# Optimization experiments

Measured on AMD Instinct MI355X. Metric: run time of the kernel, lower is better.

## Reference

```python
import jax, jax.numpy as jnp
import numpy as np

KERNEL = (7, 7)
NUM_CH = 4
EPS = 1e-06
ROPE_BASE = 10000.0


def _rel_dist():
    coords = [np.arange(k, dtype=np.float32) - k // 2 for k in KERNEL]
    g = np.meshgrid(*coords, indexing='ij')
    d = np.sqrt(sum(gi ** 2 for gi in g))
    return jnp.asarray(d.reshape(-1)), float(d.max())


def silu(x):
    return x * jax.nn.sigmoid(x)


def rmsnorm(x, w):
    rms = jnp.sqrt(jnp.mean(x * x, axis=-1, keepdims=True) + EPS)
    return x / rms * w


def apply_rope(x):
    # x: (B, L, H, D); positions run over dim -2 (matches torch default)
    H, D = x.shape[-2], x.shape[-1]
    half = D // 2
    pos = jnp.arange(H, dtype=jnp.float32)
    freqs = 1.0 / (ROPE_BASE ** (jnp.arange(half, dtype=x.dtype) / half))
    ang = pos[:, None] * freqs  # (H, half)
    cos, sin = jnp.cos(ang), jnp.sin(ang)
    x1, x2 = x[..., :half], x[..., half:2 * half]
    return jnp.concatenate([x1 * cos - x2 * sin, x1 * sin + x2 * cos], axis=-1)


def unfold2d(x):
    # x: (B, Hs, Ws, C) -> (B, Hs, Ws, k1*k2, C), row-major kernel order
    B, Hs, Ws, C = x.shape
    k1, k2 = KERNEL
    xp = jnp.pad(x, ((0, 0), ((k1 - 1) // 2, k1 // 2), ((k2 - 1) // 2, k2 // 2), (0, 0)))
    wins = [xp[:, i:i + Hs, j:j + Ws, :] for i in range(k1) for j in range(k2)]
    return jnp.stack(wins, axis=3)


def setup_inputs() -> dict:
    key = jax.random.key(0)
    ks = jax.random.split(key, 8)
    C = 256
    x = jax.random.normal(ks[0], (2, 64, 64, C), dtype=jnp.float32)
    W_qkv = jax.random.normal(ks[1], (C, 3 * C), dtype=jnp.float32) * 0.02
    w_qnorm = jnp.ones((C // NUM_CH,), dtype=jnp.float32)
    w_knorm = jnp.ones((C // NUM_CH,), dtype=jnp.float32)
    W_wp = jax.random.normal(ks[2], (C, 2 * NUM_CH), dtype=jnp.float32) * 0.02
    b_wp = jax.random.normal(ks[3], (2 * NUM_CH,), dtype=jnp.float32) * 0.02
    w_onorm = jnp.ones((C,), dtype=jnp.float32)
    W_out = jax.random.normal(ks[4], (C, C), dtype=jnp.float32) * 0.02
    W_gate = jax.random.normal(ks[5], (C, C), dtype=jnp.float32) * 0.02
    b_gate = 2.0 * jnp.ones((C,), dtype=jnp.float32)
    return {"x": x, "W_qkv": W_qkv, "w_qnorm": w_qnorm, "w_knorm": w_knorm,
            "W_wp": W_wp, "b_wp": b_wp, "w_onorm": w_onorm, "W_out": W_out,
            "W_gate": W_gate, "b_gate": b_gate}


def reference(x, W_qkv, w_qnorm, w_knorm, W_wp, b_wp, w_onorm, W_out, W_gate, b_gate):
    rel_dist, max_dist = _rel_dist()
    B, Hs, Ws, C = x.shape
    L = Hs * Ws
    H = NUM_CH
    D = C // H
    Wsz = KERNEL[0] * KERNEL[1]
    scale = D ** (-0.5)

    qkv = silu(x @ W_qkv)
    q, k, v = jnp.split(qkv, 3, axis=-1)

    q_flat = apply_rope(rmsnorm(q.reshape(B, L, H, D), w_qnorm))
    k_flat = apply_rope(rmsnorm(k.reshape(B, L, H, D), w_knorm))
    k = k_flat.reshape(B, Hs, Ws, C)

    wp = silu(x @ W_wp + b_wp)  # (B, Hs, Ws, 2H)
    width_raw, sharp_raw = jnp.split(wp, 2, axis=-1)
    width = jax.nn.sigmoid(width_raw) * max_dist + 0.5
    sharpness = jax.nn.sigmoid(sharp_raw) * 9.5 + 0.5

    k_win = unfold2d(k).reshape(B, L, Wsz, H, D)
    v_win = unfold2d(v).reshape(B, L, Wsz, H, D)

    scores = jnp.einsum('blhd,blwhd->blhw', q_flat, k_win) * scale
    width_f = width.reshape(B, L, H, 1)
    sharp_f = sharpness.reshape(B, L, H, 1)
    soft_mask = jax.nn.sigmoid((width_f - rel_dist) * sharp_f)
    scores = scores - (1.0 - soft_mask) * 10000.0
    attn = jax.nn.softmax(scores, axis=-1)

    out = jnp.einsum('blhw,blwhd->blhd', attn, v_win).reshape(B, Hs, Ws, C)
    out = rmsnorm(out, w_onorm)

    gate = jax.nn.sigmoid(silu(v @ W_gate + b_gate))
    merged = gate * v + (1.0 - gate) * out
    return silu(merged @ W_out)
```

## Files before the change

### kernel.cpp

```cpp
#include <hip/hip_runtime.h>
#include <hip/hip_fp16.h>
#include <math.h>

__device__ __forceinline__ float sigm(float x)  { return 1.0f / (1.0f + __expf(-x)); }
__device__ __forceinline__ float siluf(float x) { return x * sigm(x); }

typedef _Float16 half8  __attribute__((ext_vector_type(8)));
typedef _Float16 half4  __attribute__((ext_vector_type(4)));
typedef float    f32x4  __attribute__((ext_vector_type(4)));
typedef unsigned u32x2  __attribute__((ext_vector_type(2)));

__device__ __forceinline__ void gld16(const void* g, void* l) {
    __builtin_amdgcn_global_load_lds(
        (const __attribute__((address_space(1))) unsigned*)g,
        (__attribute__((address_space(3))) unsigned*)l, 16, 0, 0);
}

template <int N>
__device__ __forceinline__ void wait_vmcnt() {
    if constexpr (N == 0)      asm volatile("s_waitcnt vmcnt(0)" ::: "memory");
    else if constexpr (N == 3) asm volatile("s_waitcnt vmcnt(3)" ::: "memory");
    else if constexpr (N == 5) asm volatile("s_waitcnt vmcnt(5)" ::: "memory");
    else if constexpr (N == 6) asm volatile("s_waitcnt vmcnt(6)" ::: "memory");
}

template <int MI, int AMODE>
__device__ __forceinline__ void gemm_core16(
    const __half* __restrict__ A16,
    const __half* __restrict__ Bhi, const __half* __restrict__ Blo,
    int nbs, int m0, int n0, int t, int koff, f32x4 (&acc)[MI][4])
{
    __shared__ short As[2][MI * 1024], BsHi[2][4096], BsLo[2][4096];
    const int lane = t & 63, wave = t >> 6;
    const int wm = (wave >> 1) * (MI << 4), wn = (wave & 1) << 6;
    const int fr = lane & 15, fq = lane >> 4;
    constexpr int NL = MI / 2 + 4;

    auto stage = [&](int kb, int buf) {
        const int kc = (kb + koff) & 7;
#pragma unroll
        for (int hf = 0; hf < MI / 2; ++hf) {
            const int rr = wave * (MI << 3) + (hf << 4);
            size_t ga;
            if (AMODE == 0)
                ga = (((size_t)(kc * 8192 + m0 + rr)) << 5) + (lane << 3);
            else
                ga = (((size_t)(m0 + rr + (lane >> 2))) << 8) + (kc << 5) + ((lane & 3) << 3);
            gld16(A16 + ga, &As[buf][rr << 5]);
        }
#pragma unroll
        for (int hf = 0; hf < 2; ++hf) {
            const int rr = (wave << 5) + (hf << 4);
            const size_t gb = (((size_t)(kc * nbs + n0 + rr)) << 5) + (lane << 3);
            gld16(Bhi + gb, &BsHi[buf][rr << 5]);
            gld16(Blo + gb, &BsLo[buf][rr << 5]);
        }
    };

    stage(0, 0);
#pragma unroll
    for (int kb = 0; kb < 8; ++kb) {
        const int cur = kb & 1;
        if (kb < 7) {
            stage(kb + 1, cur ^ 1);
            wait_vmcnt<NL>();
        } else {
            wait_vmcnt<0>();
        }
        __builtin_amdgcn_s_barrier();

        half8 a[MI], bh[4], bl[4];
#pragma unroll
        for (int i = 0; i < MI; ++i)
            a[i] = *(const half8*)&As[cur][((wm + (i << 4) + fr) << 5) + (fq << 3)];
#pragma unroll
        for (int i = 0; i < 4; ++i) {
            const int boff = ((wn + (i << 4) + fr) << 5) + (fq << 3);
            bh[i] = *(const half8*)&BsHi[cur][boff];
            bl[i] = *(const half8*)&BsLo[cur][boff];
        }
#pragma unroll
        for (int mi = 0; mi < MI; ++mi)
#pragma unroll
            for (int ni = 0; ni < 4; ++ni) {
                acc[mi][ni] = __builtin_amdgcn_mfma_f32_16x16x32_f16(a[mi], bh[ni], acc[mi][ni], 0, 0, 0);
                acc[mi][ni] = __builtin_amdgcn_mfma_f32_16x16x32_f16(a[mi], bl[ni], acc[mi][ni], 0, 0, 0);
            }

        if (kb < 7) __builtin_amdgcn_s_barrier();
    }
}

__device__ __forceinline__ void gemm_core64(
    const __half* __restrict__ A16,
    const __half* __restrict__ Bhi, const __half* __restrict__ Blo,
    int m0, int n0, int t, int koff, f32x4 (&acc)[4])
{
    __shared__ short As[2][2048], BsHi[2][2048], BsLo[2][2048];
    const int lane = t & 63, wave = t >> 6;
    const int wm = wave << 4;
    const int fr = lane & 15, fq = lane >> 4;

    auto stage = [&](int kb, int buf) {
        const int kc = (kb + koff) & 7;
        const int rr = wave << 4;
        const size_t ga = (((size_t)(m0 + rr + (lane >> 2))) << 8) + (kc << 5) + ((lane & 3) << 3);
        gld16(A16 + ga, &As[buf][rr << 5]);
        const size_t gb = (((size_t)(kc * 256 + n0 + rr)) << 5) + (lane << 3);
        gld16(Bhi + gb, &BsHi[buf][rr << 5]);
        gld16(Blo + gb, &BsLo[buf][rr << 5]);
    };

    stage(0, 0);
#pragma unroll
    for (int kb = 0; kb < 8; ++kb) {
        const int cur = kb & 1;
        if (kb < 7) {
            stage(kb + 1, cur ^ 1);
            wait_vmcnt<3>();
        } else {
            wait_vmcnt<0>();
        }
        __builtin_amdgcn_s_barrier();

        half8 a = *(const half8*)&As[cur][((wm + fr) << 5) + (fq << 3)];
        half8 bh[4], bl[4];
#pragma unroll
        for (int ni = 0; ni < 4; ++ni) {
            const int boff = (((ni << 4) + fr) << 5) + (fq << 3);
            bh[ni] = *(const half8*)&BsHi[cur][boff];
            bl[ni] = *(const half8*)&BsLo[cur][boff];
        }
#pragma unroll
        for (int ni = 0; ni < 4; ++ni) {
            acc[ni] = __builtin_amdgcn_mfma_f32_16x16x32_f16(a, bh[ni], acc[ni], 0, 0, 0);
            acc[ni] = __builtin_amdgcn_mfma_f32_16x16x32_f16(a, bl[ni], acc[ni], 0, 0, 0);
        }

        if (kb < 7) __builtin_amdgcn_s_barrier();
    }
}

__global__ __launch_bounds__(256) void prep_kernel(
    const float* __restrict__ x, const float* __restrict__ Wqkv,
    const float* __restrict__ Wgate, const float* __restrict__ Wout,
    const float* __restrict__ Wwp, const float* __restrict__ bwp,
    __half* __restrict__ xh,
    __half* __restrict__ wqh, __half* __restrict__ wql,
    __half* __restrict__ wgh, __half* __restrict__ wgl,
    __half* __restrict__ woh, __half* __restrict__ wol,
    float* __restrict__ width, float* __restrict__ sharp)
{
    __shared__ float xs[32][260];
    const int t = threadIdx.x;
    const int blk = blockIdx.x;
    if (blk < 256) {
        const int row0 = blk << 5;
        for (int e = t; e < 2048; e += 256) {
            int r = e >> 6, cc = (e & 63) << 2;
            *(float4*)&xs[r][cc] = *(const float4*)&x[(size_t)(row0 + r) * 256 + cc];
        }
        __syncthreads();
        const int r = t >> 3, kb = t & 7;
        __half hibuf[32];
#pragma unroll
        for (int i = 0; i < 32; ++i)
            hibuf[i] = __float2half(xs[r][(kb << 5) + i]);
        const size_t ob = ((size_t)(kb * 8192 + row0 + r)) << 5;
#pragma unroll
        for (int i = 0; i < 4; ++i)
            *(int4*)&xh[ob + (i << 3)] = *(int4*)&hibuf[i << 3];
        float a0 = 0.f, a1 = 0.f, a2 = 0.f, a3 = 0.f;
#pragma unroll 4
        for (int k = 0; k < 256; k += 4) {
            a0 += xs[r][k + 0] * Wwp[(k + 0) * 8 + kb];
            a1 += xs[r][k + 1] * Wwp[(k + 1) * 8 + kb];
            a2 += xs[r][k + 2] * Wwp[(k + 2) * 8 + kb];
            a3 += xs[r][k + 3] * Wwp[(k + 3) * 8 + kb];
        }
        const float acc = (a0 + a1) + (a2 + a3);
        float s = sigm(siluf(acc + bwp[kb]));
        const int row = row0 + r;
        if (kb < 4) width[row * 4 + kb] = s * 4.242640687119285f + 0.5f;
        else        sharp[row * 4 + kb - 4] = s * 9.5f + 0.5f;
    } else {
        const float* W; __half *Whi, *Wlo; int N, nb0, ncnt;
        if (blk < 288)      { W = Wqkv;  Whi = wqh; Wlo = wql; N = 768; nb0 = (blk - 256) * 24; ncnt = 24; }
        else if (blk < 296) { W = Wgate; Whi = wgh; Wlo = wgl; N = 256; nb0 = (blk - 288) * 32; ncnt = 32; }
        else                { W = Wout;  Whi = woh; Wlo = wol; N = 256; nb0 = (blk - 296) * 32; ncnt = 32; }
        for (int j = 0; j < ncnt; ++j)
            xs[j][t] = W[(size_t)t * N + nb0 + j];
        __syncthreads();
        for (int c = t; c < ncnt * 8; c += 256) {
            const int j = c >> 3, kb = c & 7;
            __half hibuf[32], lobuf[32];
#pragma unroll
            for (int i = 0; i < 32; ++i) {
                float v = xs[j][(kb << 5) + i];
                __half hv = __float2half(v);
                hibuf[i] = hv;
                lobuf[i] = __float2half(v - __half2float(hv));
            }
            const size_t ob = ((size_t)(kb * N + nb0 + j)) << 5;
#pragma unroll
            for (int i = 0; i < 4; ++i) {
                *(int4*)&Whi[ob + (i << 3)] = *(int4*)&hibuf[i << 3];
                *(int4*)&Wlo[ob + (i << 3)] = *(int4*)&lobuf[i << 3];
            }
        }
    }
}

__global__ __launch_bounds__(256, 3) void gemm_qkv(
    const __half* __restrict__ xh,
    const __half* __restrict__ wqh, const __half* __restrict__ wql,
    const float* __restrict__ wq, const float* __restrict__ wk,
    __half* __restrict__ qh, __half* __restrict__ kh, __half* __restrict__ vh)
{
    const int t  = threadIdx.x;
    const int m0 = blockIdx.y << 6, n0 = blockIdx.x << 7;
    f32x4 acc[2][4] = {};
    gemm_core16<2, 0>(xh, wqh, wql, 768, m0, n0, t, blockIdx.y & 7, acc);

    const int lane = t & 63, wave = t >> 6;
    const int wm = (wave >> 1) << 5, wn = (wave & 1) << 6;
    const int fr = lane & 15, fq = lane >> 4;
    const int gc0 = n0 + wn;
    const int seg = gc0 >> 8;
    const int h   = (gc0 >> 6) & 3;
    const int hc0 = h << 6;

#pragma unroll
    for (int mi = 0; mi < 2; ++mi)
#pragma unroll
        for (int ni = 0; ni < 4; ++ni)
#pragma unroll
            for (int r = 0; r < 4; ++r)
                acc[mi][ni][r] = siluf(acc[mi][ni][r]);

    if (seg == 2) {
#pragma unroll
        for (int mi = 0; mi < 2; ++mi)
#pragma unroll
            for (int r = 0; r < 4; ++r) {
                const size_t row = m0 + wm + (mi << 4) + (fq << 2) + r;
#pragma unroll
                for (int ni = 0; ni < 4; ++ni)
                    vh[row * 256 + hc0 + (ni << 4) + fr] = __float2half(acc[mi][ni][r]);
            }
    } else {
        const float* wnorm = seg ? wk : wq;
        float wv[4];
#pragma unroll
        for (int ni = 0; ni < 4; ++ni) wv[ni] = wnorm[(ni << 4) + fr];
        float cs[2], sn[2];
#pragma unroll
        for (int j = 0; j < 2; ++j) {
            const int d = (j << 4) + fr;
            const float freq = powf(10000.f, -(float)d * (1.f / 32.f));
            const float ang = (float)h * freq;
            cs[j] = cosf(ang); sn[j] = sinf(ang);
        }
        __half* dstbase = (seg ? kh : qh);
#pragma unroll
        for (int mi = 0; mi < 2; ++mi)
#pragma unroll
            for (int r = 0; r < 4; ++r) {
                float ss = acc[mi][0][r] * acc[mi][0][r] + acc[mi][1][r] * acc[mi][1][r]
                         + acc[mi][2][r] * acc[mi][2][r] + acc[mi][3][r] * acc[mi][3][r];
                ss += __shfl_xor(ss, 1); ss += __shfl_xor(ss, 2);
                ss += __shfl_xor(ss, 4); ss += __shfl_xor(ss, 8);
                const float rinv = 1.f / sqrtf(ss * (1.f / 64.f) + 1e-6f);
                float xv[4];
#pragma unroll
                for (int ni = 0; ni < 4; ++ni) xv[ni] = acc[mi][ni][r] * rinv * wv[ni];
                const float o0 = xv[0] * cs[0] - xv[2] * sn[0];
                const float o2 = xv[0] * sn[0] + xv[2] * cs[0];
                const float o1 = xv[1] * cs[1] - xv[3] * sn[1];
                const float o3 = xv[1] * sn[1] + xv[3] * cs[1];
                const size_t row = m0 + wm + (mi << 4) + (fq << 2) + r;
                __half* dst = dstbase + row * 256 + hc0;
                dst[fr]      = __float2half(o0);
                dst[16 + fr] = __float2half(o1);
                dst[32 + fr] = __float2half(o2);
                dst[48 + fr] = __float2half(o3);
            }
    }
}

__global__ __launch_bounds__(256, 2) void gemm_gate(
    const __half* __restrict__ vh,
    const __half* __restrict__ wgh, const __half* __restrict__ wgl,
    const float* __restrict__ bias, const float* __restrict__ attn_o,
    const float* __restrict__ sumsq4, const float* __restrict__ w_onorm,
    __half* __restrict__ mh)
{
    const int t  = threadIdx.x;
    const int m0 = blockIdx.y << 6, n0 = blockIdx.x << 6;
    f32x4 acc[4] = {};
    gemm_core64(vh, wgh, wgl, m0, n0, t, blockIdx.y & 7, acc);

    const int lane = t & 63, wave = t >> 6;
    const int wm = wave << 4;
    const int fr = lane & 15, fq = lane >> 4;

    float rmsf[4];
#pragma unroll
    for (int r = 0; r < 4; ++r) {
        const int m = m0 + wm + (fq << 2) + r;
        float4 s4 = *(const float4*)&sumsq4[(size_t)m * 4];
        rmsf[r] = 1.f / sqrtf((s4.x + s4.y + s4.z + s4.w) * (1.f / 256.f) + 1e-6f);
    }

#pragma unroll
    for (int ni = 0; ni < 4; ++ni) {
        const int n  = n0 + (ni << 4) + fr;
        const int mb = m0 + wm + (fq << 2);
        const float bb  = bias[n];
        const float won = w_onorm[n];
#pragma unroll
        for (int r = 0; r < 4; ++r) {
            const int m = mb + r;
            const float g  = sigm(siluf(acc[ni][r] + bb));
            const float vv = __half2float(vh[(size_t)m * 256 + n]);
            const float oo = attn_o[(size_t)m * 256 + n] * rmsf[r] * won;
            mh[(size_t)m * 256 + n] = __float2half(g * vv + (1.f - g) * oo);
        }
    }
}

__global__ __launch_bounds__(256, 2) void gemm_out(
    const __half* __restrict__ mh,
    const __half* __restrict__ woh, const __half* __restrict__ wol,
    float* __restrict__ out)
{
    const int t  = threadIdx.x;
    const int m0 = blockIdx.y << 6, n0 = blockIdx.x << 6;
    f32x4 acc[4] = {};
    gemm_core64(mh, woh, wol, m0, n0, t, blockIdx.y & 7, acc);

    const int lane = t & 63, wave = t >> 6;
    const int wm = wave << 4;
    const int fr = lane & 15, fq = lane >> 4;
#pragma unroll
    for (int ni = 0; ni < 4; ++ni) {
        const int n  = n0 + (ni << 4) + fr;
        const int mb = m0 + wm + (fq << 2);
#pragma unroll
        for (int r = 0; r < 4; ++r)
            out[(size_t)(mb + r) * 256 + n] = siluf(acc[ni][r]);
    }
}

#define PT 216

__global__ __launch_bounds__(256, 2) void attn_mfma(
    const __half* __restrict__ qh, const __half* __restrict__ kh,
    const __half* __restrict__ vh, const float* __restrict__ width,
    const float* __restrict__ sharp, float* __restrict__ attn_o,
    float* __restrict__ sumsq4)
{
    __shared__ short smem[27648];
    short* Ksh = smem;
    short* Psh = smem;
    short* Vt  = smem + 13824;

    const int t = threadIdx.x;
    const int lane = t & 63, wave = t >> 6;
    const int fr = lane & 15, fq = lane >> 4;
    const int patch = blockIdx.x, h = blockIdx.y, b = blockIdx.z;
    const int pr0 = (patch >> 3) << 3, pc0 = (patch & 7) << 3;
    const int t0 = (wave * 28) >> 4;

    float wd[4], sh[4]; int lq[4];
#pragma unroll
    for (int r = 0; r < 4; ++r) {
        const int q = (wave << 4) + (fq << 2) + r;
        lq[r] = (pr0 + (q >> 3)) * 64 + pc0 + (q & 7);
        wd[r] = width[((b << 12) + lq[r]) * 4 + h];
        sh[r] = sharp[((b << 12) + lq[r]) * 4 + h];
    }

    const int qrow = (wave << 4) + fr;
    const int lqr = (pr0 + (qrow >> 3)) * 64 + pc0 + (qrow & 7);
    const __half* qptr = qh + (((size_t)(b << 12) + lqr) << 8) + (h << 6) + (fq << 3);
    half8 a0 = *(const half8*)qptr;
    half8 a1 = *(const half8*)(qptr + 32);

    const int srow = t >> 4;
    const int d4 = (t & 15) << 2;
    const size_t cbase = (((size_t)b << 12) * 256) + (size_t)h * 64 + d4;

    u32x2 kb2[13], vb2[13];
#pragma unroll
    for (int p = 0; p < 13; ++p) {
        const int prow = (p << 4) + srow;
        const int pi = prow / 14, pj = prow - pi * 14;
        const int gr = pr0 - 3 + pi, gc = pc0 - 3 + pj;
        const bool ok = (prow < 196) & ((unsigned)gr < 64u) & ((unsigned)gc < 64u);
        const int grc = min(max(gr, 0), 63), gcc = min(max(gc, 0), 63);
        const size_t off = cbase + (size_t)(grc * 64 + gcc) * 256;
        u32x2 kv = *(const u32x2*)(kh + off);
        u32x2 vv = *(const u32x2*)(vh + off);
        const u32x2 z = {0u, 0u};
        kb2[p] = ok ? kv : z;
        vb2[p] = ok ? vv : z;
    }

    const int chunk = d4 >> 3, dlo = d4 & 7;
#pragma unroll
    for (int p = 0; p < 13; ++p) {
        const int prow = (p << 4) + srow;
        *(u32x2*)&Ksh[(prow << 6) + ((chunk ^ (prow & 7)) << 3) + dlo] = kb2[p];
        Vt[(d4)     * PT + prow] = (short)(vb2[p].x & 0xffffu);
        Vt[(d4 + 1) * PT + prow] = (short)(vb2[p].x >> 16);
        Vt[(d4 + 2) * PT + prow] = (short)(vb2[p].y & 0xffffu);
        Vt[(d4 + 3) * PT + prow] = (short)(vb2[p].y >> 16);
    }
    __syncthreads();

    f32x4 sc[8];
#pragma unroll
    for (int tl = 0; tl < 8; ++tl) {
        const int kr = ((t0 + tl) << 4) + fr;
        half8 b0 = *(const half8*)&Ksh[(kr << 6) + (((0 + fq) ^ (kr & 7)) << 3)];
        half8 b1 = *(const half8*)&Ksh[(kr << 6) + (((4 + fq) ^ (kr & 7)) << 3)];
        f32x4 z = {0.f, 0.f, 0.f, 0.f};
        z = __builtin_amdgcn_mfma_f32_16x16x32_f16(a0, b0, z, 0, 0, 0);
        sc[tl] = __builtin_amdgcn_mfma_f32_16x16x32_f16(a1, b1, z, 0, 0, 0);
    }

    float mx[4] = {-3e38f, -3e38f, -3e38f, -3e38f};
#pragma unroll
    for (int tl = 0; tl < 8; ++tl) {
        const int p = ((t0 + tl) << 4) + fr;
        const int pi = p / 14, pj = p - pi * 14;
        const bool pvld = p < 196;
#pragma unroll
        for (int r = 0; r < 4; ++r) {
            const int q = (wave << 4) + (fq << 2) + r;
            const int di = pi - 3 - ((q >> 3) & 7), dj = pj - 3 - (q & 7);
            const bool win = pvld & ((unsigned)(di + 3) <= 6u) & ((unsigned)(dj + 3) <= 6u);
            const float rel = sqrtf((float)(di * di + dj * dj));
            const float mk = sigm((wd[r] - rel) * sh[r]);
            float s = sc[tl][r] * 0.125f - (1.f - mk) * 10000.f;
            s = win ? s : -3e38f;
            sc[tl][r] = s;
            mx[r] = fmaxf(mx[r], s);
        }
    }
#pragma unroll
    for (int r = 0; r < 4; ++r) {
        mx[r] = fmaxf(mx[r], __shfl_xor(mx[r], 1));
        mx[r] = fmaxf(mx[r], __shfl_xor(mx[r], 2));
        mx[r] = fmaxf(mx[r], __shfl_xor(mx[r], 4));
        mx[r] = fmaxf(mx[r], __shfl_xor(mx[r], 8));
    }
    float sm[4] = {0.f, 0.f, 0.f, 0.f};
#pragma unroll
    for (int tl = 0; tl < 8; ++tl)
#pragma unroll
        for (int r = 0; r < 4; ++r) {
            const float e = __expf(sc[tl][r] - mx[r]);
            sc[tl][r] = e; sm[r] += e;
        }
#pragma unroll
    for (int r = 0; r < 4; ++r) {
        sm[r] += __shfl_xor(sm[r], 1);
        sm[r] += __shfl_xor(sm[r], 2);
        sm[r] += __shfl_xor(sm[r], 4);
        sm[r] += __shfl_xor(sm[r], 8);
        sm[r] = 1.f / sm[r];
    }

    __syncthreads();
#pragma unroll
    for (int tl = 0; tl < 8; ++tl)
#pragma unroll
        for (int r = 0; r < 4; ++r) {
            __half pv = __float2half(sc[tl][r] * sm[r]);
            Psh[((wave << 4) + (fq << 2) + r) * PT + ((t0 + tl) << 4) + fr] = *(short*)&pv;
        }
    asm volatile("s_waitcnt lgkmcnt(0)" ::: "memory");
    __builtin_amdgcn_sched_barrier(0);

    f32x4 o[4] = {};
    const int pra = (wave << 4) + fr;
    const int cb = t0 << 4;
#pragma unroll
    for (int s = 0; s < 4; ++s) {
        half8 pa = *(const half8*)&Psh[pra * PT + cb + (fq << 3) + (s << 5)];
#pragma unroll
        for (int dt = 0; dt < 4; ++dt) {
            half8 vbf = *(const half8*)&Vt[((dt << 4) + fr) * PT + cb + (fq << 3) + (s << 5)];
            o[dt] = __builtin_amdgcn_mfma_f32_16x16x32_f16(pa, vbf, o[dt], 0, 0, 0);
        }
    }

#pragma unroll
    for (int r = 0; r < 4; ++r) {
        float ss = o[0][r]*o[0][r] + o[1][r]*o[1][r] + o[2][r]*o[2][r] + o[3][r]*o[3][r];
        ss += __shfl_xor(ss, 1); ss += __shfl_xor(ss, 2);
        ss += __shfl_xor(ss, 4); ss += __shfl_xor(ss, 8);
        const size_t rowb = (((size_t)(b << 12) + lq[r]) << 8) + h * 64;
#pragma unroll
        for (int dt = 0; dt < 4; ++dt)
            attn_o[rowb + (dt << 4) + fr] = o[dt][r];
        if (fr == 0) sumsq4[(((b << 12) + lq[r]) << 2) + h] = ss;
    }
}

extern "C" void kernel_launch(void* const* d_in, const int* in_sizes, int n_in,
                              void* d_out, int out_size, void* d_ws, size_t ws_size,
                              hipStream_t stream)
{
    const float* x      = (const float*)d_in[0];
    const float* W_qkv  = (const float*)d_in[1];
    const float* w_qn   = (const float*)d_in[2];
    const float* w_kn   = (const float*)d_in[3];
    const float* W_wp   = (const float*)d_in[4];
    const float* b_wp   = (const float*)d_in[5];
    const float* w_on   = (const float*)d_in[6];
    const float* W_out  = (const float*)d_in[7];
    const float* W_gate = (const float*)d_in[8];
    const float* b_gate = (const float*)d_in[9];
    float* out = (float*)d_out;

    __half* ws16 = (__half*)d_ws;
    __half* xh  = ws16;
    __half* wqh = xh  + 2097152;
    __half* wql = wqh + 196608;
    __half* wgh = wql + 196608;
    __half* wgl = wgh + 65536;
    __half* woh = wgl + 65536;
    __half* wol = woh + 65536;
    __half* qhp = wol + 65536;
    __half* khp = qhp + 2097152;
    __half* vhp = khp + 2097152;
    __half* mh  = vhp + 2097152;
    float* attn_o = (float*)(mh + 2097152);
    float* widthp = attn_o + 2097152;
    float* sharpp = widthp + 32768;
    float* sumsq4 = sharpp + 32768;

    prep_kernel<<<304, 256, 0, stream>>>(x, W_qkv, W_gate, W_out, W_wp, b_wp,
                                         xh, wqh, wql, wgh, wgl, woh, wol,
                                         widthp, sharpp);
    gemm_qkv<<<dim3(6, 128), 256, 0, stream>>>(xh, wqh, wql, w_qn, w_kn,
                                               qhp, khp, vhp);
    attn_mfma<<<dim3(64, 4, 2), 256, 0, stream>>>(qhp, khp, vhp, widthp, sharpp,
                                                  attn_o, sumsq4);
    gemm_gate<<<dim3(4, 128), 256, 0, stream>>>(vhp, wgh, wgl, b_gate,
                                                attn_o, sumsq4, w_on, mh);
    gemm_out<<<dim3(4, 128), 256, 0, stream>>>(mh, woh, wol, out);
}
```

Measured before the change: 132.6 us.

## Co-schedule gate GEMM with attention blocks and fuse merge into output GEMM

The gate GEMM now runs as extra blocks inside the attention launch, sharing its LDS buffer, so both execute concurrently in one grid and the launch count drops. It writes raw fp32 gate pre-activations instead of a merged fp16 tensor. The merge step (sigmoid gate, RMS-normalised attention output, blend with v) moves into the prologue of the output GEMM, which builds the fp16 A tile directly in LDS. This removes one kernel launch and the round trip of the merged tensor, at the cost of writing and reading an extra fp32 buffer and a heavier, less pipelined prologue in the output GEMM.

```diff
diff --git a/kernel.cpp b/kernel.cpp
--- a/kernel.cpp
+++ b/kernel.cpp
@@ -19,6 +19,7 @@
 template <int N>
 __device__ __forceinline__ void wait_vmcnt() {
     if constexpr (N == 0)      asm volatile("s_waitcnt vmcnt(0)" ::: "memory");
+    else if constexpr (N == 2) asm volatile("s_waitcnt vmcnt(2)" ::: "memory");
     else if constexpr (N == 3) asm volatile("s_waitcnt vmcnt(3)" ::: "memory");
     else if constexpr (N == 5) asm volatile("s_waitcnt vmcnt(5)" ::: "memory");
     else if constexpr (N == 6) asm volatile("s_waitcnt vmcnt(6)" ::: "memory");
@@ -91,12 +92,15 @@
     }
 }
 
-__device__ __forceinline__ void gemm_core64(
+__device__ __forceinline__ void gemm_core64_lds(
+    short* lds,
     const __half* __restrict__ A16,
     const __half* __restrict__ Bhi, const __half* __restrict__ Blo,
     int m0, int n0, int t, int koff, f32x4 (&acc)[4])
 {
-    __shared__ short As[2][2048], BsHi[2][2048], BsLo[2][2048];
+    short* As   = lds;
+    short* BsHi = lds + 4096;
+    short* BsLo = lds + 8192;
     const int lane = t & 63, wave = t >> 6;
     const int wm = wave << 4;
     const int fr = lane & 15, fq = lane >> 4;
@@ -105,10 +109,10 @@
         const int kc = (kb + koff) & 7;
         const int rr = wave << 4;
         const size_t ga = (((size_t)(m0 + rr + (lane >> 2))) << 8) + (kc << 5) + ((lane & 3) << 3);
-        gld16(A16 + ga, &As[buf][rr << 5]);
+        gld16(A16 + ga, &As[buf * 2048 + (rr << 5)]);
         const size_t gb = (((size_t)(kc * 256 + n0 + rr)) << 5) + (lane << 3);
-        gld16(Bhi + gb, &BsHi[buf][rr << 5]);
-        gld16(Blo + gb, &BsLo[buf][rr << 5]);
+        gld16(Bhi + gb, &BsHi[buf * 2048 + (rr << 5)]);
+        gld16(Blo + gb, &BsLo[buf * 2048 + (rr << 5)]);
     };
 
     stage(0, 0);
@@ -123,13 +127,13 @@
         }
         __builtin_amdgcn_s_barrier();
 
-        half8 a = *(const half8*)&As[cur][((wm + fr) << 5) + (fq << 3)];
+        half8 a = *(const half8*)&As[cur * 2048 + ((wm + fr) << 5) + (fq << 3)];
         half8 bh[4], bl[4];
 #pragma unroll
         for (int ni = 0; ni < 4; ++ni) {
             const int boff = (((ni << 4) + fr) << 5) + (fq << 3);
-            bh[ni] = *(const half8*)&BsHi[cur][boff];
-            bl[ni] = *(const half8*)&BsLo[cur][boff];
+            bh[ni] = *(const half8*)&BsHi[cur * 2048 + boff];
+            bl[ni] = *(const half8*)&BsLo[cur * 2048 + boff];
         }
 #pragma unroll
         for (int ni = 0; ni < 4; ++ni) {
@@ -288,87 +292,45 @@
     }
 }
 
-__global__ __launch_bounds__(256, 2) void gemm_gate(
-    const __half* __restrict__ vh,
-    const __half* __restrict__ wgh, const __half* __restrict__ wgl,
-    const float* __restrict__ bias, const float* __restrict__ attn_o,
-    const float* __restrict__ sumsq4, const float* __restrict__ w_onorm,
-    __half* __restrict__ mh)
-{
-    const int t  = threadIdx.x;
-    const int m0 = blockIdx.y << 6, n0 = blockIdx.x << 6;
-    f32x4 acc[4] = {};
-    gemm_core64(vh, wgh, wgl, m0, n0, t, blockIdx.y & 7, acc);
-
-    const int lane = t & 63, wave = t >> 6;
-    const int wm = wave << 4;
-    const int fr = lane & 15, fq = lane >> 4;
-
-    float rmsf[4];
-#pragma unroll
-    for (int r = 0; r < 4; ++r) {
-        const int m = m0 + wm + (fq << 2) + r;
-        float4 s4 = *(const float4*)&sumsq4[(size_t)m * 4];
-        rmsf[r] = 1.f / sqrtf((s4.x + s4.y + s4.z + s4.w) * (1.f / 256.f) + 1e-6f);
-    }
-
-#pragma unroll
-    for (int ni = 0; ni < 4; ++ni) {
-        const int n  = n0 + (ni << 4) + fr;
-        const int mb = m0 + wm + (fq << 2);
-        const float bb  = bias[n];
-        const float won = w_onorm[n];
-#pragma unroll
-        for (int r = 0; r < 4; ++r) {
-            const int m = mb + r;
-            const float g  = sigm(siluf(acc[ni][r] + bb));
-            const float vv = __half2float(vh[(size_t)m * 256 + n]);
-            const float oo = attn_o[(size_t)m * 256 + n] * rmsf[r] * won;
-            mh[(size_t)m * 256 + n] = __float2half(g * vv + (1.f - g) * oo);
-        }
-    }
-}
-
-__global__ __launch_bounds__(256, 2) void gemm_out(
-    const __half* __restrict__ mh,
-    const __half* __restrict__ woh, const __half* __restrict__ wol,
-    float* __restrict__ out)
-{
-    const int t  = threadIdx.x;
-    const int m0 = blockIdx.y << 6, n0 = blockIdx.x << 6;
-    f32x4 acc[4] = {};
-    gemm_core64(mh, woh, wol, m0, n0, t, blockIdx.y & 7, acc);
-
-    const int lane = t & 63, wave = t >> 6;
-    const int wm = wave << 4;
-    const int fr = lane & 15, fq = lane >> 4;
-#pragma unroll
-    for (int ni = 0; ni < 4; ++ni) {
-        const int n  = n0 + (ni << 4) + fr;
-        const int mb = m0 + wm + (fq << 2);
-#pragma unroll
-        for (int r = 0; r < 4; ++r)
-            out[(size_t)(mb + r) * 256 + n] = siluf(acc[ni][r]);
-    }
-}
-
 #define PT 216
 
-__global__ __launch_bounds__(256, 2) void attn_mfma(
+__global__ __launch_bounds__(256, 2) void attn_gate(
     const __half* __restrict__ qh, const __half* __restrict__ kh,
     const __half* __restrict__ vh, const float* __restrict__ width,
-    const float* __restrict__ sharp, float* __restrict__ attn_o,
-    float* __restrict__ sumsq4)
+    const float* __restrict__ sharp,
+    const __half* __restrict__ wgh, const __half* __restrict__ wgl,
+    float* __restrict__ attn_o, float* __restrict__ sumsq4,
+    float* __restrict__ graw)
 {
     __shared__ short smem[27648];
+    const int bid = blockIdx.x;
+    const int t = threadIdx.x;
+    const int lane = t & 63, wave = t >> 6;
+    const int fr = lane & 15, fq = lane >> 4;
+
+    if (bid >= 512) {
+        const int gid = bid - 512;
+        const int n0 = (gid & 3) << 6;
+        const int m0 = (gid >> 2) << 6;
+        f32x4 acc[4] = {};
+        gemm_core64_lds(smem, vh, wgh, wgl, m0, n0, t, (gid >> 2) & 7, acc);
+        const int wm = wave << 4;
+#pragma unroll
+        for (int ni = 0; ni < 4; ++ni) {
+            const int n  = n0 + (ni << 4) + fr;
+            const int mb = m0 + wm + (fq << 2);
+#pragma unroll
+            for (int r = 0; r < 4; ++r)
+                graw[(size_t)(mb + r) * 256 + n] = acc[ni][r];
+        }
+        return;
+    }
+
     short* Ksh = smem;
     short* Psh = smem;
     short* Vt  = smem + 13824;
 
-    const int t = threadIdx.x;
-    const int lane = t & 63, wave = t >> 6;
-    const int fr = lane & 15, fq = lane >> 4;
-    const int patch = blockIdx.x, h = blockIdx.y, b = blockIdx.z;
+    const int patch = bid & 63, h = (bid >> 6) & 3, b = bid >> 8;
     const int pr0 = (patch >> 3) << 3, pc0 = (patch & 7) << 3;
     const int t0 = (wave * 28) >> 4;
 
@@ -507,6 +469,100 @@
         for (int dt = 0; dt < 4; ++dt)
             attn_o[rowb + (dt << 4) + fr] = o[dt][r];
         if (fr == 0) sumsq4[(((b << 12) + lq[r]) << 2) + h] = ss;
+    }
+}
+
+__global__ __launch_bounds__(256, 3) void gemm_mergeout(
+    const float* __restrict__ graw, const __half* __restrict__ vh,
+    const float* __restrict__ attn_o, const float* __restrict__ sumsq4,
+    const float* __restrict__ w_onorm, const float* __restrict__ bias,
+    const __half* __restrict__ woh, const __half* __restrict__ wol,
+    float* __restrict__ out)
+{
+    __shared__ short Ash[64 * 264];
+    __shared__ short BsHi[2][2048], BsLo[2][2048];
+
+    const int t = threadIdx.x;
+    const int lane = t & 63, wave = t >> 6;
+    const int fr = lane & 15, fq = lane >> 4;
+    const int m0 = blockIdx.y << 6, n0 = blockIdx.x << 6;
+    const int koff = blockIdx.y & 7;
+
+    auto stageB = [&](int kb, int buf) {
+        const int kc = (kb + koff) & 7;
+        const int rr = wave << 4;
+        const size_t gb = (((size_t)(kc * 256 + n0 + rr)) << 5) + (lane << 3);
+        gld16(woh + gb, &BsHi[buf][rr << 5]);
+        gld16(wol + gb, &BsLo[buf][rr << 5]);
+    };
+
+    stageB(0, 0);
+
+    for (int e = t; e < 4096; e += 256) {
+        const int row = e >> 6;
+        const int c4  = (e & 63) << 2;
+        const int m = m0 + row;
+        float4 s4 = *(const float4*)&sumsq4[(size_t)m * 4];
+        const float rms = 1.f / sqrtf((s4.x + s4.y + s4.z + s4.w) * (1.f / 256.f) + 1e-6f);
+        float4 gr = *(const float4*)&graw[(size_t)m * 256 + c4];
+        float4 ao = *(const float4*)&attn_o[(size_t)m * 256 + c4];
+        float4 wn = *(const float4*)&w_onorm[c4];
+        float4 bb = *(const float4*)&bias[c4];
+        u32x2 vv2 = *(const u32x2*)(vh + (size_t)m * 256 + c4);
+        const __half* vvh = (const __half*)&vv2;
+        __half mg[4];
+        {
+            const float g0 = sigm(siluf(gr.x + bb.x));
+            mg[0] = __float2half(g0 * __half2float(vvh[0]) + (1.f - g0) * (ao.x * rms * wn.x));
+            const float g1 = sigm(siluf(gr.y + bb.y));
+            mg[1] = __float2half(g1 * __half2float(vvh[1]) + (1.f - g1) * (ao.y * rms * wn.y));
+            const float g2 = sigm(siluf(gr.z + bb.z));
+            mg[2] = __float2half(g2 * __half2float(vvh[2]) + (1.f - g2) * (ao.z * rms * wn.z));
+            const float g3 = sigm(siluf(gr.w + bb.w));
+            mg[3] = __float2half(g3 * __half2float(vvh[3]) + (1.f - g3) * (ao.w * rms * wn.w));
+        }
+        *(u32x2*)&Ash[row * 264 + c4] = *(u32x2*)mg;
+    }
+    __syncthreads();
+
+    f32x4 acc[4] = {};
+    const int wm = wave << 4;
+#pragma unroll
+    for (int kb = 0; kb < 8; ++kb) {
+        const int cur = kb & 1;
+        if (kb < 7) {
+            stageB(kb + 1, cur ^ 1);
+            wait_vmcnt<2>();
+        } else {
+            wait_vmcnt<0>();
+        }
+        __builtin_amdgcn_s_barrier();
+
+        const int kc = (kb + koff) & 7;
+        half8 a = *(const half8*)&Ash[(wm + fr) * 264 + (kc << 5) + (fq << 3)];
+        half8 bh[4], bl[4];
+#pragma unroll
+        for (int ni = 0; ni < 4; ++ni) {
+            const int boff = (((ni << 4) + fr) << 5) + (fq << 3);
+            bh[ni] = *(const half8*)&BsHi[cur][boff];
+            bl[ni] = *(const half8*)&BsLo[cur][boff];
+        }
+#pragma unroll
+        for (int ni = 0; ni < 4; ++ni) {
+            acc[ni] = __builtin_amdgcn_mfma_f32_16x16x32_f16(a, bh[ni], acc[ni], 0, 0, 0);
+            acc[ni] = __builtin_amdgcn_mfma_f32_16x16x32_f16(a, bl[ni], acc[ni], 0, 0, 0);
+        }
+
+        if (kb < 7) __builtin_amdgcn_s_barrier();
+    }
+
+#pragma unroll
+    for (int ni = 0; ni < 4; ++ni) {
+        const int n  = n0 + (ni << 4) + fr;
+        const int mb = m0 + wm + (fq << 2);
+#pragma unroll
+        for (int r = 0; r < 4; ++r)
+            out[(size_t)(mb + r) * 256 + n] = siluf(acc[ni][r]);
     }
 }
 
@@ -537,20 +593,19 @@
     __half* qhp = wol + 65536;
     __half* khp = qhp + 2097152;
     __half* vhp = khp + 2097152;
-    __half* mh  = vhp + 2097152;
-    float* attn_o = (float*)(mh + 2097152);
+    float* attn_o = (float*)(vhp + 2097152);
     float* widthp = attn_o + 2097152;
     float* sharpp = widthp + 32768;
     float* sumsq4 = sharpp + 32768;
+    float* graw   = sumsq4 + 32768;
 
     prep_kernel<<<304, 256, 0, stream>>>(x, W_qkv, W_gate, W_out, W_wp, b_wp,
                                          xh, wqh, wql, wgh, wgl, woh, wol,
                                          widthp, sharpp);
     gemm_qkv<<<dim3(6, 128), 256, 0, stream>>>(xh, wqh, wql, w_qn, w_kn,
                                                qhp, khp, vhp);
-    attn_mfma<<<dim3(64, 4, 2), 256, 0, stream>>>(qhp, khp, vhp, widthp, sharpp,
-                                                  attn_o, sumsq4);
-    gemm_gate<<<dim3(4, 128), 256, 0, stream>>>(vhp, wgh, wgl, b_gate,
-                                                attn_o, sumsq4, w_on, mh);
-    gemm_out<<<dim3(4, 128), 256, 0, stream>>>(mh, woh, wol, out);
-}
+    attn_gate<<<1024, 256, 0, stream>>>(qhp, khp, vhp, widthp, sharpp,
+                                        wgh, wgl, attn_o, sumsq4, graw);
+    gemm_mergeout<<<dim3(4, 128), 256, 0, stream>>>(graw, vhp, attn_o, sumsq4,
+                                                    w_on, b_gate, woh, wol, out);
+}
```

New measurement: 139.4 us. 5.2% more time.
